# Kernel optimization log

Hardware: AMD Instinct MI355X
Metric: run time of the kernel (lower is better)

## Reference

```python
import jax, jax.numpy as jnp
import numpy as np

T = 400      # timestamps (window length chosen == timestamps -> no padding branch)
D = 10000    # out_dimension (HDC hypervector dim)
TWO_PI = 2.0 * np.pi


def setup_inputs() -> dict:
    key = jax.random.key(0)
    ks = jax.random.split(key, 10)
    # monotonically increasing timestamps so jerk dt > 0
    t = jnp.cumsum(jax.random.uniform(ks[0], (T,), jnp.float32) + 0.5)
    xyz = jax.random.normal(ks[1], (T, 3), jnp.float32)
    inp = jnp.concatenate([t[:, None], xyz], axis=1)  # [T,4] = (t, x, y, z)
    W1 = jax.random.normal(ks[2], (D, T * 3), jnp.float32)
    b1 = jax.random.uniform(ks[3], (D,), jnp.float32, 0.0, TWO_PI)
    W2 = jax.random.normal(ks[4], (D, T * 3), jnp.float32)
    b2 = jax.random.uniform(ks[5], (D,), jnp.float32, 0.0, TWO_PI)
    W3 = jax.random.normal(ks[6], (D, T * 2), jnp.float32)
    b3 = jax.random.uniform(ks[7], (D,), jnp.float32, 0.0, TWO_PI)
    W4 = jax.random.normal(ks[8], (D, 3), jnp.float32)
    b4 = jax.random.uniform(ks[9], (D,), jnp.float32, 0.0, TWO_PI)
    return {"input": inp, "W1": W1, "b1": b1, "W2": W2, "b2": b2,
            "W3": W3, "b3": b3, "W4": W4, "b4": b4}


def _hypertangent(x, W, b):
    # HyperTangent random-feature embedding: tanh(W @ x + b)
    return jnp.tanh(W @ x + b)


def reference(input, W1, b1, W2, b2, W3, b3, W4, b4):
    t = input[:, 0] - input[0, 0]           # zero-base the time column
    xyz = input[:, 1:]                      # [T,3]
    sq = xyz * xyz
    mags = jnp.sqrt(jnp.sum(sq, axis=1))    # [T]
    energy = jnp.sum(sq, axis=0) / xyz.shape[0]  # [3]
    # vectorized jerk: (x_{i+1}-x_i)/(t_{i+1}-t_i), with a leading zeros row
    dt = (t[1:] - t[:-1])[:, None]          # [T-1,1]
    jerks = jnp.concatenate(
        [jnp.zeros((1, 3), input.dtype), (xyz[1:] - xyz[:-1]) / dt], axis=0)  # [T,3]
    jerk_mags = jnp.sqrt(jnp.sum(jerks * jerks, axis=1))  # [T]
    # window == timestamps -> no padding path
    features1 = jnp.concatenate([xyz[:, 0], xyz[:, 1], xyz[:, 2]])      # [3T]
    features2 = jnp.concatenate([jerks[:, 0], jerks[:, 1], jerks[:, 2]])  # [3T]
    features3 = jnp.concatenate([mags, jerk_mags])                       # [2T]
    hv1 = _hypertangent(features1, W1, b1)
    hv2 = _hypertangent(features2, W2, b2)
    hv3 = _hypertangent(features3, W3, b3)
    hv4 = _hypertangent(energy, W4, b4)
    return jnp.tanh(hv1 * hv4 + hv2 + hv3)  # [D]
```

## Files before the change

kernel.cpp:

```cpp
#include <hip/hip_runtime.h>
#include <hip/hip_bf16.h>
#include <math.h>

#define T_PTS 400
#define D_OUT 10000
#define L12   1200
#define L3    800

#define FEAT_F 3328
#define PART_OFF 3328
#define WS_NEED ((FEAT_F + 16 * D_OUT) * sizeof(float))

__global__ __launch_bounds__(512)
void hdc_features_kernel(const float* __restrict__ in, float* __restrict__ feat) {
    __shared__ float red[3][8];
    const int tid = threadIdx.x;
    float ex = 0.f, ey = 0.f, ez = 0.f;

    if (tid < T_PTS) {
        const float4 cur = reinterpret_cast<const float4*>(in)[tid];
        const float x = cur.y, y = cur.z, z = cur.w;
        feat[tid]        = x;
        feat[400 + tid]  = y;
        feat[800 + tid]  = z;
        feat[2400 + tid] = sqrtf(x * x + y * y + z * z);
        ex = x * x; ey = y * y; ez = z * z;

        float jx = 0.f, jy = 0.f, jz = 0.f;
        if (tid > 0) {
            const float4 prev = reinterpret_cast<const float4*>(in)[tid - 1];
            const float dt = cur.x - prev.x;
            const float inv = 1.0f / dt;
            jx = (x - prev.y) * inv;
            jy = (y - prev.z) * inv;
            jz = (z - prev.w) * inv;
        }
        feat[1200 + tid] = jx;
        feat[1600 + tid] = jy;
        feat[2000 + tid] = jz;
        feat[2800 + tid] = sqrtf(jx * jx + jy * jy + jz * jz);
    }

    #pragma unroll
    for (int off = 32; off; off >>= 1) {
        ex += __shfl_down(ex, off, 64);
        ey += __shfl_down(ey, off, 64);
        ez += __shfl_down(ez, off, 64);
    }
    const int wave = tid >> 6, lane = tid & 63;
    if (lane == 0) { red[0][wave] = ex; red[1][wave] = ey; red[2][wave] = ez; }
    __syncthreads();
    if (tid == 0) {
        float sx = 0.f, sy = 0.f, sz = 0.f;
        #pragma unroll
        for (int w = 0; w < 8; ++w) { sx += red[0][w]; sy += red[1][w]; sz += red[2][w]; }
        const float invT = 1.0f / (float)T_PTS;
        feat[3200] = sx * invT;
        feat[3201] = sy * invT;
        feat[3202] = sz * invT;
    }
}

__global__ __launch_bounds__(256)
void hdc_dot_kernel(const float* __restrict__ W1, const float* __restrict__ W2,
                    const float* __restrict__ W3, const float* __restrict__ feat,
                    float* __restrict__ partial) {
    const int wid = blockIdx.x * 4 + (threadIdx.x >> 6);
    const int lane = threadIdx.x & 63;

    const float* __restrict__ Wm;
    int row, c, len, foff, slot;
    if (wid < 50000) {
        Wm = W1; row = wid / 5; c = wid - row * 5; len = L12; foff = 0; slot = c;
    } else if (wid < 100000) {
        const int u = wid - 50000;
        Wm = W2; row = u / 5; c = u - row * 5; len = L12; foff = 1200; slot = 5 + c;
    } else {
        const int u = wid - 100000;
        Wm = W3; row = u / 4; c = u - row * 4; len = L3; foff = 2400; slot = 10 + c;
    }

    const int k = c * 256 + lane * 4;
    float t = 0.f;
    if (k < len) {
        const float4 w = *reinterpret_cast<const float4*>(Wm + (size_t)row * len + k);
        const float4 f = *reinterpret_cast<const float4*>(feat + foff + k);
        t = w.x * f.x + w.y * f.y + w.z * f.z + w.w * f.w;
    }
    #pragma unroll
    for (int off = 32; off; off >>= 1) t += __shfl_down(t, off, 64);
    if (lane == 0) partial[row * 16 + slot] = t;
}

__global__ __launch_bounds__(256)
void hdc_tanh_kernel(const float* __restrict__ partial,
                     const float* __restrict__ b1, const float* __restrict__ b2,
                     const float* __restrict__ b3, const float* __restrict__ W4,
                     const float* __restrict__ b4, const float* __restrict__ feat,
                     float* __restrict__ out) {
    const int d = blockIdx.x * 256 + threadIdx.x;
    if (d >= D_OUT) return;
    const float* __restrict__ p = partial + d * 16;
    const float a1 = ((p[0] + p[1]) + (p[2] + p[3])) + p[4];
    const float a2 = ((p[5] + p[6]) + (p[7] + p[8])) + p[9];
    const float a3 = (p[10] + p[11]) + (p[12] + p[13]);
    const float e0 = feat[3200], e1 = feat[3201], e2 = feat[3202];
    const float hv1 = tanhf(a1 + b1[d]);
    const float hv2 = tanhf(a2 + b2[d]);
    const float hv3 = tanhf(a3 + b3[d]);
    const float hv4 = tanhf(W4[(size_t)d * 3 + 0] * e0 +
                            W4[(size_t)d * 3 + 1] * e1 +
                            W4[(size_t)d * 3 + 2] * e2 + b4[d]);
    out[d] = tanhf(hv1 * hv4 + hv2 + hv3);
}

__global__ __launch_bounds__(256)
void hdc_gemv_fallback(const float* __restrict__ W1, const float* __restrict__ b1,
                       const float* __restrict__ W2, const float* __restrict__ b2,
                       const float* __restrict__ W3, const float* __restrict__ b3,
                       const float* __restrict__ W4, const float* __restrict__ b4,
                       const float* __restrict__ feat, float* __restrict__ out) {
    __shared__ __align__(16) float g[3203];
    const int tid = threadIdx.x;
    const int wave = tid >> 6, lane = tid & 63;
    const int d = blockIdx.x * 4 + wave;
    const int c0 = lane * 4;

    const float* __restrict__ w1 = W1 + (size_t)d * L12;
    const float* __restrict__ w2 = W2 + (size_t)d * L12;
    const float* __restrict__ w3 = W3 + (size_t)d * L3;

    float4 r[12];
    #pragma unroll
    for (int i = 0; i < 12; ++i) {
        const int k = 256 * i + c0;
        const float* p;
        if (i < 4)       p = w1 + k;
        else if (i == 4) p = (k < L12) ? (w1 + k) : (w2 + (k - L12));
        else if (i < 9)  p = w2 + (k - L12);
        else if (i == 9) p = (k < 2400) ? (w2 + (k - L12)) : (w3 + (k - 2400));
        else             p = w3 + (k - 2400);
        r[i] = *reinterpret_cast<const float4*>(p);
    }
    const float2 rt = *reinterpret_cast<const float2*>(w3 + 672 + 2 * lane);

    {
        float4* g4 = reinterpret_cast<float4*>(g);
        const float4* feat4 = reinterpret_cast<const float4*>(feat);
        for (int i = tid; i < 800; i += 256) g4[i] = feat4[i];
        if (tid == 0) { g[3200] = feat[3200]; g[3201] = feat[3201]; g[3202] = feat[3202]; }
    }
    __syncthreads();

    float acc1 = 0.f, acc2 = 0.f, acc3 = 0.f;
    #pragma unroll
    for (int i = 0; i < 12; ++i) {
        const int k = 256 * i + c0;
        const float4 s = *reinterpret_cast<const float4*>(&g[k]);
        const float t = r[i].x * s.x + r[i].y * s.y + r[i].z * s.z + r[i].w * s.w;
        if (i < 4)       acc1 += t;
        else if (i == 4) { acc1 += (k < L12) ? t : 0.f; acc2 += (k < L12) ? 0.f : t; }
        else if (i < 9)  acc2 += t;
        else if (i == 9) { acc2 += (k < 2400) ? t : 0.f; acc3 += (k < 2400) ? 0.f : t; }
        else             acc3 += t;
    }
    {
        const int k = 3072 + 2 * lane;
        acc3 += rt.x * g[k] + rt.y * g[k + 1];
    }

    #pragma unroll
    for (int off = 32; off; off >>= 1) {
        acc1 += __shfl_down(acc1, off, 64);
        acc2 += __shfl_down(acc2, off, 64);
        acc3 += __shfl_down(acc3, off, 64);
    }

    if (lane == 0) {
        const float e0 = g[3200], e1 = g[3201], e2 = g[3202];
        const float hv1 = tanhf(acc1 + b1[d]);
        const float hv2 = tanhf(acc2 + b2[d]);
        const float hv3 = tanhf(acc3 + b3[d]);
        const float hv4 = tanhf(W4[(size_t)d * 3 + 0] * e0 +
                                W4[(size_t)d * 3 + 1] * e1 +
                                W4[(size_t)d * 3 + 2] * e2 + b4[d]);
        out[d] = tanhf(hv1 * hv4 + hv2 + hv3);
    }
}

extern "C" void kernel_launch(void* const* d_in, const int* in_sizes, int n_in,
                              void* d_out, int out_size, void* d_ws, size_t ws_size,
                              hipStream_t stream) {
    const float* input = (const float*)d_in[0];
    const float* W1 = (const float*)d_in[1];
    const float* b1 = (const float*)d_in[2];
    const float* W2 = (const float*)d_in[3];
    const float* b2 = (const float*)d_in[4];
    const float* W3 = (const float*)d_in[5];
    const float* b3 = (const float*)d_in[6];
    const float* W4 = (const float*)d_in[7];
    const float* b4 = (const float*)d_in[8];
    float* out = (float*)d_out;
    float* feat = (float*)d_ws;

    hdc_features_kernel<<<1, 512, 0, stream>>>(input, feat);

    if (ws_size >= WS_NEED) {
        float* partial = feat + PART_OFF;
        hdc_dot_kernel<<<35000, 256, 0, stream>>>(W1, W2, W3, feat, partial);
        hdc_tanh_kernel<<<(D_OUT + 255) / 256, 256, 0, stream>>>(
            partial, b1, b2, b3, W4, b4, feat, out);
    } else {
        hdc_gemv_fallback<<<D_OUT / 4, 256, 0, stream>>>(W1, b1, W2, b2, W3, b3,
                                                         W4, b4, feat, out);
    }
}
```

Before: 164.7 us.

## Use persistent waves computing full row dots instead of per-chunk waves

Replaces the 35000-block kernel, where each wave handled one 256-element chunk of a row, with a 1024-block grid-stride kernel in which each wave computes a whole row dot product and issues up to five float4 loads per lane. The partial buffer shrinks to one value per (matrix,row), and the tanh kernel reads three values instead of summing 14 partials. This cuts block launch overhead and partial-sum traffic while keeping more loads in flight per wave. The trade-off is a fixed grid of 4096 waves that may not saturate memory bandwidth, plus idle lanes on the W3 rows' last chunk.

```diff
diff --git a/kernel.cpp b/kernel.cpp
--- a/kernel.cpp
+++ b/kernel.cpp
@@ -6,10 +6,11 @@
 #define D_OUT 10000
 #define L12   1200
 #define L3    800
-
-#define FEAT_F 3328
+#define N_TASKS 30000
+#define N_WAVES 4096
+
 #define PART_OFF 3328
-#define WS_NEED ((FEAT_F + 16 * D_OUT) * sizeof(float))
+#define WS_NEED ((3328 + N_TASKS) * sizeof(float))
 
 __global__ __launch_bounds__(512)
 void hdc_features_kernel(const float* __restrict__ in, float* __restrict__ feat) {
@@ -61,35 +62,44 @@
     }
 }
 
-__global__ __launch_bounds__(256)
-void hdc_dot_kernel(const float* __restrict__ W1, const float* __restrict__ W2,
-                    const float* __restrict__ W3, const float* __restrict__ feat,
-                    float* __restrict__ partial) {
-    const int wid = blockIdx.x * 4 + (threadIdx.x >> 6);
+__global__ __launch_bounds__(256, 4)
+void hdc_dot_pipe(const float* __restrict__ W1, const float* __restrict__ W2,
+                  const float* __restrict__ W3, const float* __restrict__ feat,
+                  float* __restrict__ partial) {
+    const int wv   = blockIdx.x * 4 + (threadIdx.x >> 6);
     const int lane = threadIdx.x & 63;
-
-    const float* __restrict__ Wm;
-    int row, c, len, foff, slot;
-    if (wid < 50000) {
-        Wm = W1; row = wid / 5; c = wid - row * 5; len = L12; foff = 0; slot = c;
-    } else if (wid < 100000) {
-        const int u = wid - 50000;
-        Wm = W2; row = u / 5; c = u - row * 5; len = L12; foff = 1200; slot = 5 + c;
-    } else {
-        const int u = wid - 100000;
-        Wm = W3; row = u / 4; c = u - row * 4; len = L3; foff = 2400; slot = 10 + c;
-    }
-
-    const int k = c * 256 + lane * 4;
-    float t = 0.f;
-    if (k < len) {
-        const float4 w = *reinterpret_cast<const float4*>(Wm + (size_t)row * len + k);
-        const float4 f = *reinterpret_cast<const float4*>(feat + foff + k);
-        t = w.x * f.x + w.y * f.y + w.z * f.z + w.w * f.w;
-    }
-    #pragma unroll
-    for (int off = 32; off; off >>= 1) t += __shfl_down(t, off, 64);
-    if (lane == 0) partial[row * 16 + slot] = t;
+    const int c0   = lane * 4;
+    const float4 z4 = make_float4(0.f, 0.f, 0.f, 0.f);
+
+    for (int t = wv; t < N_TASKS; t += N_WAVES) {
+        const int m   = (t >= 20000) ? 2 : ((t >= 10000) ? 1 : 0);
+        const int row = t - m * 10000;
+        const float* __restrict__ Wm = (m == 0) ? W1 : ((m == 1) ? W2 : W3);
+        const int len = (m == 2) ? L3 : L12;
+        const float* __restrict__ wr = Wm + (size_t)row * len;
+        const float* __restrict__ fr = feat + m * 1200;
+
+        float4 r[5], s[5];
+        #pragma unroll
+        for (int i = 0; i < 5; ++i) {
+            const int k = c0 + 256 * i;
+            r[i] = (k < len) ? *reinterpret_cast<const float4*>(wr + k) : z4;
+        }
+        #pragma unroll
+        for (int i = 0; i < 5; ++i) {
+            const int k = c0 + 256 * i;
+            s[i] = (k < len) ? *reinterpret_cast<const float4*>(fr + k) : z4;
+        }
+
+        float a = 0.f;
+        #pragma unroll
+        for (int i = 0; i < 5; ++i)
+            a += r[i].x * s[i].x + r[i].y * s[i].y + r[i].z * s[i].z + r[i].w * s[i].w;
+
+        #pragma unroll
+        for (int off = 32; off; off >>= 1) a += __shfl_down(a, off, 64);
+        if (lane == 0) partial[t] = a;
+    }
 }
 
 __global__ __launch_bounds__(256)
@@ -100,10 +110,9 @@
                      float* __restrict__ out) {
     const int d = blockIdx.x * 256 + threadIdx.x;
     if (d >= D_OUT) return;
-    const float* __restrict__ p = partial + d * 16;
-    const float a1 = ((p[0] + p[1]) + (p[2] + p[3])) + p[4];
-    const float a2 = ((p[5] + p[6]) + (p[7] + p[8])) + p[9];
-    const float a3 = (p[10] + p[11]) + (p[12] + p[13]);
+    const float a1 = partial[d];
+    const float a2 = partial[10000 + d];
+    const float a3 = partial[20000 + d];
     const float e0 = feat[3200], e1 = feat[3201], e2 = feat[3202];
     const float hv1 = tanhf(a1 + b1[d]);
     const float hv2 = tanhf(a2 + b2[d]);
@@ -207,7 +216,7 @@
 
     if (ws_size >= WS_NEED) {
         float* partial = feat + PART_OFF;
-        hdc_dot_kernel<<<35000, 256, 0, stream>>>(W1, W2, W3, feat, partial);
+        hdc_dot_pipe<<<N_WAVES / 4, 256, 0, stream>>>(W1, W2, W3, feat, partial);
         hdc_tanh_kernel<<<(D_OUT + 255) / 256, 256, 0, stream>>>(
             partial, b1, b2, b3, W4, b4, feat, out);
     } else {
```

Measured after the change: 168.6 us. 2.4% more time.
